# Performance work log

Hardware: AMD Instinct MI355X
Metric: run time of the kernel (lower is better)

Reference implementation:

```python
import jax, jax.numpy as jnp
import numpy as np

BN_EPS = 1e-5
STRIDE = 8  # encoder output stride -> upsample target is H*8


def conv2d(x, w, pad):
    return jax.lax.conv_general_dilated(
        x, w, (1, 1), [(pad, pad), (pad, pad)],
        dimension_numbers=('NCHW', 'OIHW', 'NCHW'))


def batchnorm(x, gamma, beta):
    # training-mode BN (batch statistics), matching a freshly-constructed torch module
    m = jnp.mean(x, axis=(0, 2, 3), keepdims=True)
    v = jnp.var(x, axis=(0, 2, 3), keepdims=True)
    xn = (x - m) * jax.lax.rsqrt(v + BN_EPS)
    return xn * gamma[None, :, None, None] + beta[None, :, None, None]


def setup_inputs() -> dict:
    key = jax.random.key(0)
    ks = jax.random.split(key, 8)
    B, C, H, W = 8, 256, 60, 60
    NC = 2
    return {
        'V_a': jax.random.normal(ks[0], (B, C, H, W), jnp.float32),
        'V_b': jax.random.normal(ks[1], (B, C, H, W), jnp.float32),
        'W_sim': jax.random.normal(ks[2], (C, C), jnp.float32) * 0.02,
        'gate_w': jax.random.normal(ks[3], (1, C, 1, 1), jnp.float32) * 0.01,
        'convA_w': jax.random.normal(ks[4], (C, 2 * C, 3, 3), jnp.float32) * 0.01,
        'convB_w': jax.random.normal(ks[5], (C, 2 * C, 3, 3), jnp.float32) * 0.01,
        'bnA_gamma': jnp.ones((C,), jnp.float32),
        'bnA_beta': jnp.zeros((C,), jnp.float32),
        'bnB_gamma': jnp.ones((C,), jnp.float32),
        'bnB_beta': jnp.zeros((C,), jnp.float32),
        'clsA_w': jax.random.normal(ks[6], (NC, C, 1, 1), jnp.float32) * 0.01,
        'clsA_b': jnp.zeros((NC,), jnp.float32),
        'clsB_w': jax.random.normal(ks[7], (NC, C, 1, 1), jnp.float32) * 0.01,
        'clsB_b': jnp.zeros((NC,), jnp.float32),
    }


def reference(V_a, V_b, W_sim, gate_w, convA_w, convB_w,
              bnA_gamma, bnA_beta, bnB_gamma, bnB_beta,
              clsA_w, clsA_b, clsB_w, clsB_b):
    B, C, H, W = V_a.shape
    HW = H * W
    out_h, out_w = H * STRIDE, W * STRIDE

    Va = V_a.reshape(B, C, HW)  # [B,C,HW_a]
    Vb = V_b.reshape(B, C, HW)  # [B,C,HW_b]

    # Linear on V_a^T: out[b,i,d] = sum_c Va[b,c,i] * W_sim[d,c]
    WVa = jnp.einsum('dc,bci->bdi', W_sim, Va)           # [B,C,HW_a]
    S = jnp.einsum('bdi,bdj->bij', WVa, Vb)              # [B,HW_a,HW_b]

    S_row = jax.nn.softmax(S, axis=1)                    # softmax over a-positions
    A_col = jax.nn.softmax(S, axis=2)                    # softmax over b-positions

    Z_b = jnp.einsum('bci,bij->bcj', Va, S_row).reshape(B, C, H, W)
    Z_a = jnp.einsum('bcj,bij->bci', Vb, A_col).reshape(B, C, H, W)

    mask_a = jax.nn.sigmoid(conv2d(Z_a, gate_w, 0))
    mask_b = jax.lax.stop_gradient(jax.nn.sigmoid(conv2d(Z_b, gate_w, 0)))
    Z_a = Z_a * mask_a
    Z_b = Z_b * mask_b

    Z_a = jnp.concatenate([Z_a, V_a], axis=1)            # [B,2C,H,W]
    Z_b = jnp.concatenate([Z_b, V_b], axis=1)

    Z_a = jax.nn.relu(batchnorm(conv2d(Z_a, convA_w, 1), bnA_gamma, bnA_beta))
    Z_b = jax.nn.relu(batchnorm(conv2d(Z_b, convB_w, 1), bnB_gamma, bnB_beta))

    x1 = conv2d(Z_a, clsA_w, 0) + clsA_b[None, :, None, None]
    x2 = conv2d(Z_b, clsB_w, 0) + clsB_b[None, :, None, None]

    NC = x1.shape[1]
    x1 = jax.image.resize(x1, (B, NC, out_h, out_w), method='bilinear')
    x2 = jax.image.resize(x2, (B, NC, out_h, out_w), method='bilinear')

    return jnp.stack([jax.nn.sigmoid(x1), jax.nn.sigmoid(x2)])  # [2,B,NC,out_h,out_w]
```

## Files before the change

kernel.cpp:

```cpp
#include <hip/hip_runtime.h>

#define C_CH   256
#define BATCH  8
#define HW     3600
#define CHW    (C_CH*HW)
#define NPIX   (BATCH*HW)
#define KCONV  4608
#define OHW    480
#define KP     3648
#define NROWP  3712
#define XPIX   3844
#define NT     57

typedef __attribute__((ext_vector_type(8))) short s16x8;
typedef __attribute__((ext_vector_type(4))) float f32x4;

__device__ __forceinline__ unsigned short f2bf(float f){
  unsigned int u = __float_as_uint(f);
  u += 0x7FFF + ((u>>16)&1);
  return (unsigned short)(u>>16);
}

__device__ __forceinline__ void gload16(const void* g, void* l){
  __builtin_amdgcn_global_load_lds((const __attribute__((address_space(1))) void*)g,
                                   (__attribute__((address_space(3))) void*)l, 16, 0, 0);
}

__device__ __forceinline__ void gemm_core(const char* a0, const char* b0,
                                          size_t lda, size_t ldb, int nkt,
                                          f32x4 acc[4][4]){
  __shared__ __align__(16) char LDS[32768];
  const int tid = threadIdx.x, l = tid & 63, w = tid >> 6;
  char* AsW = LDS + w*1024;
  char* BsW = LDS + 16384 + w*1024;
  const int arow = (w>>1)*64 + (l&15);
  const int brow = (w&1)*64 + (l&15);
  const int kc0 = (((l>>4)*16)      ) ^ ((l&7)<<4);
  const int kc1 = (((l>>4)*16) + 64 ) ^ ((l&7)<<4);
  const char* Ab = LDS;
  const char* Bb = LDS + 16384;
  for (int kt = 0; kt < nkt; ++kt){
#pragma unroll
    for (int i=0;i<4;i++){
      gload16(a0 + (size_t)(i*32)*lda + (size_t)kt*128, AsW + i*4096);
      gload16(b0 + (size_t)(i*32)*ldb + (size_t)kt*128, BsW + i*4096);
    }
    asm volatile("s_waitcnt vmcnt(0)" ::: "memory");
    __syncthreads();
    s16x8 af[4][2], bf[4][2];
#pragma unroll
    for (int f=0;f<4;f++){
      af[f][0] = *(const s16x8*)(Ab + (arow+f*16)*128 + kc0);
      af[f][1] = *(const s16x8*)(Ab + (arow+f*16)*128 + kc1);
      bf[f][0] = *(const s16x8*)(Bb + (brow+f*16)*128 + kc0);
      bf[f][1] = *(const s16x8*)(Bb + (brow+f*16)*128 + kc1);
    }
#pragma unroll
    for (int ks=0;ks<2;ks++)
#pragma unroll
      for (int fm=0;fm<4;fm++)
#pragma unroll
        for (int fn=0;fn<4;fn++)
          acc[fm][fn] = __builtin_amdgcn_mfma_f32_16x16x32_bf16(af[fm][ks], bf[fn][ks], acc[fm][fn], 0,0,0);
    __syncthreads();
  }
}

__global__ __launch_bounds__(256) void k_gemm_wva(const unsigned short* __restrict__ VaT,
                                                  const unsigned short* __restrict__ Wsim16,
                                                  unsigned short* __restrict__ WVaT){
  const int tid = threadIdx.x, l = tid&63, w = tid>>6;
  const int b = blockIdx.z;
  const int n0 = blockIdx.x*128, m0 = blockIdx.y*128;
  const int colS = ((tid&7)*16) ^ (((tid>>3)&7)<<4);
  const char* a0 = (const char*)(VaT + (size_t)b*NROWP*256) + (size_t)(m0 + (tid>>3))*512 + colS;
  const char* b0 = (const char*)Wsim16 + (size_t)(n0 + (tid>>3))*512 + colS;
  f32x4 acc[4][4] = {};
  gemm_core(a0, b0, 512, 512, 4, acc);
  unsigned short* ob = WVaT + (size_t)b*NROWP*256;
  const int mb = m0 + (w>>1)*64 + (l>>4)*4;
  const int nb = n0 + (w&1)*64 + (l&15);
#pragma unroll
  for (int fm=0;fm<4;fm++)
#pragma unroll
    for (int fn=0;fn<4;fn++){
      int n = nb + fn*16;
#pragma unroll
      for (int r=0;r<4;r++){
        int m = mb + fm*16 + r;
        if (m < HW) ob[(size_t)m*256 + n] = f2bf(acc[fm][fn][r]);
      }
    }
}

__global__ __launch_bounds__(256, 3) void flash_attn(const char* __restrict__ WVaT,
                                                  const char* __restrict__ VbT,
                                                  const char* __restrict__ VaT,
                                                  const char* __restrict__ Va16,
                                                  const char* __restrict__ Vb16,
                                                  const float* __restrict__ gw,
                                                  unsigned short* __restrict__ XtA,
                                                  unsigned short* __restrict__ XtB){
  __shared__ __align__(16) char LDS[40960];
  const int tid = threadIdx.x, l = tid&63, w = tid>>6;
  const int b = blockIdx.y, side = blockIdx.z;
  const size_t tOff = (size_t)b*NROWP*512;
  const size_t vOff = (size_t)b*256*KP*2;
  const char* QT = (side ? VbT  : WVaT) + tOff;
  const char* Kt = (side ? WVaT : VbT ) + tOff;
  const char* Vp = (side ? Va16 : Vb16) + vOff;
  const char* Vc = (side ? VbT  : VaT ) + tOff;
  unsigned short* Xt = (side ? XtB : XtA) + (size_t)b*XPIX*512;
  const int i0 = blockIdx.x*64;

  char* Kls = LDS;
  char* Pls = LDS + 32768;

  s16x8 q[8];
  {
    const char* qp = QT + (size_t)(i0 + w*16 + (l&15))*512 + (l>>4)*16;
#pragma unroll
    for (int ks=0;ks<8;ks++) q[ks] = *(const s16x8*)(qp + ks*64);
  }
  float gwv[4];
#pragma unroll
  for (int fn=0;fn<4;fn++) gwv[fn] = gw[w*64 + fn*16 + (l&15)];

  f32x4 acc[4][4] = {};
  f32x4 lac = {0.f,0.f,0.f,0.f};

  auto stageK = [&](int t){
    const char* src = Kt + (size_t)t*32768;
#pragma unroll
    for (int p=0;p<8;p++){
      int row = p*8 + (tid>>5), ch = tid&31;
      gload16(src + (size_t)row*512 + ((ch*16) ^ ((row&7)<<4)), Kls + p*4096 + tid*16);
    }
  };

  stageK(0);
  asm volatile("s_waitcnt vmcnt(0)" ::: "memory");
  __syncthreads();

  const char* vrow = Vp + (size_t)(w*64 + (l&15))*(KP*2) + (l>>4)*16;
  const int g = l>>4;

  for (int t=0; t<NT; ++t){
    s16x8 bv[2][4];
#pragma unroll
    for (int ks=0;ks<2;ks++)
#pragma unroll
      for (int fn=0;fn<4;fn++)
        bv[ks][fn] = *(const s16x8*)(vrow + (size_t)fn*16*(KP*2) + (size_t)t*128 + ks*64);
    f32x4 sac[4] = {};
#pragma unroll
    for (int ks=0;ks<8;ks++){
      s16x8 bk[4];
#pragma unroll
      for (int fn=0;fn<4;fn++){
        int row = fn*16 + (l&15);
        bk[fn] = *(const s16x8*)(Kls + row*512 + ((ks*64 + (l>>4)*16) ^ ((row&7)<<4)));
      }
#pragma unroll
      for (int fn=0;fn<4;fn++)
        sac[fn] = __builtin_amdgcn_mfma_f32_16x16x32_bf16(q[ks], bk[fn], sac[fn], 0,0,0);
    }
    const int j0 = t*64;
#pragma unroll
    for (int fn=0;fn<4;fn++){
      int col = fn*16 + (l&15);
      bool jv = (j0 + col) < HW;
#pragma unroll
      for (int r=0;r<4;r++){
        float e = jv ? __expf(sac[fn][r]) : 0.f;
        lac[r] += e;
        int row = w*16 + g*4 + r;
        *(unsigned short*)(Pls + row*128 + ((col*2) ^ (g<<5))) = f2bf(e);
      }
    }
    __syncthreads();
    if (t+1 < NT) stageK(t+1);
#pragma unroll
    for (int ks=0;ks<2;ks++){
      s16x8 ap[4];
#pragma unroll
      for (int fm=0;fm<4;fm++){
        int row = fm*16 + (l&15);
        ap[fm] = *(const s16x8*)(Pls + row*128 + ((ks*64 + (l>>4)*16) ^ ((((l&15)>>2)&3)<<5)));
      }
#pragma unroll
      for (int fm=0;fm<4;fm++)
#pragma unroll
        for (int fn=0;fn<4;fn++)
          acc[fm][fn] = __builtin_amdgcn_mfma_f32_16x16x32_bf16(ap[fm], bv[ks][fn], acc[fm][fn], 0,0,0);
    }
    asm volatile("s_waitcnt vmcnt(0)" ::: "memory");
    __syncthreads();
  }

  float* Lred = (float*)(LDS + 32768);
  float* Mls  = Lred + 64;
  float* Gp   = Mls + 64;
#pragma unroll
  for (int r=0;r<4;r++){
    float v = lac[r];
    v += __shfl_xor(v,1); v += __shfl_xor(v,2); v += __shfl_xor(v,4); v += __shfl_xor(v,8);
    if ((l&15)==0) Lred[w*16 + (l>>4)*4 + r] = 1.f / v;
  }
  __syncthreads();
#pragma unroll
  for (int fm=0;fm<4;fm++){
#pragma unroll
    for (int r=0;r<4;r++){
      float v = acc[fm][0][r]*gwv[0] + acc[fm][1][r]*gwv[1]
              + acc[fm][2][r]*gwv[2] + acc[fm][3][r]*gwv[3];
      v += __shfl_xor(v,1); v += __shfl_xor(v,2); v += __shfl_xor(v,4); v += __shfl_xor(v,8);
      if ((l&15)==0) Gp[w*64 + fm*16 + (l>>4)*4 + r] = v;
    }
  }
  __syncthreads();
  if (tid < 64){
    float gt = (Gp[tid] + Gp[64+tid] + Gp[128+tid] + Gp[192+tid]) * Lred[tid];
    Mls[tid] = 1.f/(1.f + __expf(-gt));
  }
  __syncthreads();
  char* Ost = LDS;
#pragma unroll
  for (int fm=0;fm<4;fm++){
    float4 li = *(const float4*)&Lred[fm*16 + (l>>4)*4];
    float4 mk = *(const float4*)&Mls [fm*16 + (l>>4)*4];
    float s0 = li.x*mk.x, s1 = li.y*mk.y, s2 = li.z*mk.z, s3 = li.w*mk.w;
#pragma unroll
    for (int fn=0;fn<4;fn++){
      int col = w*64 + fn*16 + (l&15);
      int row = fm*16 + (l>>4)*4;
      *(unsigned short*)(Ost + (row+0)*512 + col*2) = f2bf(acc[fm][fn][0]*s0);
      *(unsigned short*)(Ost + (row+1)*512 + col*2) = f2bf(acc[fm][fn][1]*s1);
      *(unsigned short*)(Ost + (row+2)*512 + col*2) = f2bf(acc[fm][fn][2]*s2);
      *(unsigned short*)(Ost + (row+3)*512 + col*2) = f2bf(acc[fm][fn][3]*s3);
    }
  }
  __syncthreads();
  {
    int row = tid>>2, ch = tid&3;
    int p = i0 + row;
    if (p < HW){
      int y = p/60, x = p - y*60;
      char* dst = (char*)Xt + (size_t)((y+1)*62 + (x+1))*1024 + ch*128;
      const char* osrc = Ost + row*512 + ch*128;
      const char* vsrc = Vc + (size_t)p*512 + ch*128;
#pragma unroll
      for (int q8=0;q8<8;q8++) *(uint4*)(dst + q8*16) = *(const uint4*)(osrc + q8*16);
#pragma unroll
      for (int q8=0;q8<8;q8++) *(uint4*)(dst + 512 + q8*16) = *(const uint4*)(vsrc + q8*16);
    }
  }
}

__global__ __launch_bounds__(256) void k_gemm_conv(const unsigned short* __restrict__ WcA,
                                                   const unsigned short* __restrict__ WcB,
                                                   const unsigned short* __restrict__ XtA,
                                                   const unsigned short* __restrict__ XtB,
                                                   float* __restrict__ Ra, float* __restrict__ Rb){
  __shared__ __align__(16) char LDS[32768];
  const int tid = threadIdx.x, l = tid&63, w = tid>>6;
  const unsigned short* Wc = blockIdx.z ? WcB : WcA;
  const unsigned short* Xt = blockIdx.z ? XtB : XtA;
  float* R = blockIdx.z ? Rb : Ra;
  const int n0 = blockIdx.x*128, m0 = blockIdx.y*128;
  const int colS = ((tid&7)*16) ^ (((tid>>3)&7)<<4);
  const int srow = tid>>3;
  const char* a0 = (const char*)Wc + (size_t)(m0+srow)*(KCONV*2) + colS;
  size_t bbase[4];
#pragma unroll
  for (int i=0;i<4;i++){
    int n = n0 + i*32 + srow;
    int bb = n/HW, p = n - bb*HW;
    int y = p/60, x = p - y*60;
    bbase[i] = ((size_t)bb*XPIX + (size_t)(y+1)*62 + (x+1))*1024 + colS;
  }
  char* AsW = LDS + w*1024;
  char* BsW = LDS + 16384 + w*1024;
  const int arow = (w>>1)*64 + (l&15);
  const int brow = (w&1)*64 + (l&15);
  const int kc0 = (((l>>4)*16)      ) ^ ((l&7)<<4);
  const int kc1 = (((l>>4)*16) + 64 ) ^ ((l&7)<<4);
  const char* Ab = LDS;
  const char* Bb = LDS + 16384;
  f32x4 acc[4][4] = {};
  for (int kt = 0; kt < 72; ++kt){
    const int sh = kt>>3;
    const int ci0b = (kt&7)*128;
    const int dy = sh/3 - 1, dx = (sh - (sh/3)*3) - 1;
    const int boff = (dy*62 + dx)*1024 + ci0b;
#pragma unroll
    for (int i=0;i<4;i++){
      gload16(a0 + (size_t)(i*32)*(KCONV*2) + (size_t)kt*128, AsW + i*4096);
      gload16((const char*)Xt + bbase[i] + boff, BsW + i*4096);
    }
    asm volatile("s_waitcnt vmcnt(0)" ::: "memory");
    __syncthreads();
    s16x8 af[4][2], bfr[4][2];
#pragma unroll
    for (int f=0;f<4;f++){
      af[f][0]  = *(const s16x8*)(Ab + (arow+f*16)*128 + kc0);
      af[f][1]  = *(const s16x8*)(Ab + (arow+f*16)*128 + kc1);
      bfr[f][0] = *(const s16x8*)(Bb + (brow+f*16)*128 + kc0);
      bfr[f][1] = *(const s16x8*)(Bb + (brow+f*16)*128 + kc1);
    }
#pragma unroll
    for (int ks=0;ks<2;ks++)
#pragma unroll
      for (int fm=0;fm<4;fm++)
#pragma unroll
        for (int fn=0;fn<4;fn++)
          acc[fm][fn] = __builtin_amdgcn_mfma_f32_16x16x32_bf16(af[fm][ks], bfr[fn][ks], acc[fm][fn], 0,0,0);
    __syncthreads();
  }
  const int mb = m0 + (w>>1)*64 + (l>>4)*4;
  const int nb = n0 + (w&1)*64 + (l&15);
#pragma unroll
  for (int fm=0;fm<4;fm++)
#pragma unroll
    for (int fn=0;fn<4;fn++){
      int n = nb + fn*16;
      int bb = n/HW, p = n - bb*HW;
      float* op = R + (size_t)bb*CHW + (size_t)(mb+fm*16)*HW + p;
#pragma unroll
      for (int r=0;r<4;r++) op[(size_t)r*HW] = acc[fm][fn][r];
    }
}

__global__ __launch_bounds__(256) void zerok(uint4* __restrict__ p, int n){
  int i = blockIdx.x*256 + threadIdx.x;
  if (i < n) p[i] = make_uint4(0,0,0,0);
}

__global__ __launch_bounds__(256) void convert_bf16(const float* __restrict__ in, unsigned short* __restrict__ out, int n){
  int i = blockIdx.x*256 + threadIdx.x;
  if (i < n) out[i] = f2bf(in[i]);
}

__global__ __launch_bounds__(256) void convw(const float* __restrict__ in, unsigned short* __restrict__ out){
  int idx = blockIdx.x*256 + threadIdx.x;
  int co = idx / KCONV;
  int kp = idx - co*KCONV;
  int sh = kp >> 9, ci = kp & 511;
  out[idx] = f2bf(in[co*KCONV + ci*9 + sh]);
}

__global__ __launch_bounds__(256) void convv(const float* __restrict__ in, unsigned short* __restrict__ out){
  int idx = blockIdx.x*256 + threadIdx.x;
  int row = idx / KP;
  int k = idx - row*KP;
  out[idx] = (k < HW) ? f2bf(in[(size_t)row*HW + k]) : 0;
}

__global__ __launch_bounds__(256) void convt(const float* __restrict__ in, unsigned short* __restrict__ out){
  __shared__ unsigned short T[64][66];
  const int b = blockIdx.y;
  const int i0 = blockIdx.x*64;
  const float* inb = in + (size_t)b*CHW;
  unsigned short* ob = out + (size_t)b*NROWP*256;
  for (int cc=0; cc<4; ++cc){
    __syncthreads();
    int i = i0 + (threadIdx.x & 63);
    int ic = i < HW ? i : HW-1;
#pragma unroll
    for (int r=0;r<16;r++){
      int cl = (threadIdx.x>>6)*16 + r;
      T[cl][threadIdx.x & 63] = f2bf(inb[(size_t)(cc*64+cl)*HW + ic]);
    }
    __syncthreads();
    int il = threadIdx.x>>2, seg = threadIdx.x&3;
    unsigned short tmp[16];
#pragma unroll
    for (int e=0;e<16;e++) tmp[e] = T[seg*16+e][il];
    *(s16x8*)(ob + (size_t)(i0+il)*256 + cc*64 + seg*16)     = *(const s16x8*)tmp;
    *(s16x8*)(ob + (size_t)(i0+il)*256 + cc*64 + seg*16 + 8) = *(const s16x8*)(tmp+8);
  }
}

__global__ __launch_bounds__(256) void bn_stats(const float* __restrict__ X, float* __restrict__ sums){
  int co = blockIdx.x;
  float s = 0.f, ss = 0.f;
  for (int i = threadIdx.x; i < NPIX; i += 256){
    int bi = i / HW, p = i - bi*HW;
    float v = X[(size_t)bi*CHW + (size_t)co*HW + p];
    s += v; ss += v*v;
  }
  __shared__ float rs[256], rss[256];
  rs[threadIdx.x] = s; rss[threadIdx.x] = ss; __syncthreads();
  for (int off=128; off>0; off>>=1){
    if (threadIdx.x < off){ rs[threadIdx.x] += rs[threadIdx.x+off]; rss[threadIdx.x] += rss[threadIdx.x+off]; }
    __syncthreads();
  }
  if (threadIdx.x==0){ sums[co] = rs[0]; sums[256+co] = rss[0]; }
}

__global__ __launch_bounds__(256) void cls_kernel(const float* __restrict__ R, const float* __restrict__ sums,
                                                  const float* __restrict__ gamma, const float* __restrict__ beta,
                                                  const float* __restrict__ cw, const float* __restrict__ cb,
                                                  float* __restrict__ Xout){
  __shared__ float red[2][4][64];
  int tx = threadIdx.x & 63, ty = threadIdx.x >> 6;
  int n = blockIdx.x*64 + tx;
  int bi = n / HW, p = n - bi*HW;
  float a0 = 0.f, a1 = 0.f;
  const float invN = 1.f/28800.f;
  for (int c = ty*64; c < ty*64+64; ++c){
    float mean = sums[c]*invN;
    float var  = sums[256+c]*invN - mean*mean;
    float sc   = gamma[c]*rsqrtf(var + 1e-5f);
    float shv  = beta[c] - mean*sc;
    float v = R[(size_t)bi*CHW + (size_t)c*HW + p]*sc + shv;
    v = fmaxf(v, 0.f);
    a0 += v*cw[c]; a1 += v*cw[256+c];
  }
  red[0][ty][tx] = a0; red[1][ty][tx] = a1; __syncthreads();
  if (ty==0){
    float r0 = red[0][0][tx]+red[0][1][tx]+red[0][2][tx]+red[0][3][tx] + cb[0];
    float r1 = red[1][0][tx]+red[1][1][tx]+red[1][2][tx]+red[1][3][tx] + cb[1];
    Xout[((size_t)bi*2 + 0)*HW + p] = r0;
    Xout[((size_t)bi*2 + 1)*HW + p] = r1;
  }
}

__global__ __launch_bounds__(256) void resize_kernel(const float* __restrict__ X1, const float* __restrict__ X2,
                                                     float* __restrict__ Out){
  int idx = blockIdx.x*256 + threadIdx.x;
  int ox = idx % OHW; int t = idx / OHW;
  int oy = t % OHW;  t /= OHW;
  int nc = t & 1;    t >>= 1;
  int bi = t & 7;    int s = t >> 3;
  const float* X = (s == 0) ? X1 : X2;
  float fy = (oy + 0.5f)*0.125f - 0.5f;
  float fx = (ox + 0.5f)*0.125f - 0.5f;
  float y0f = floorf(fy), x0f = floorf(fx);
  float wy = fy - y0f, wx = fx - x0f;
  int y0 = (int)y0f, x0 = (int)x0f;
  int y1 = min(max(y0+1,0),59), x1 = min(max(x0+1,0),59);
  y0 = min(max(y0,0),59); x0 = min(max(x0,0),59);
  const float* Xp = X + ((size_t)bi*2 + nc)*HW;
  float v00 = Xp[y0*60+x0], v01 = Xp[y0*60+x1];
  float v10 = Xp[y1*60+x0], v11 = Xp[y1*60+x1];
  float v = v00*(1.f-wy)*(1.f-wx) + v01*(1.f-wy)*wx + v10*wy*(1.f-wx) + v11*wy*wx;
  Out[idx] = 1.f/(1.f+__expf(-v));
}

extern "C" void kernel_launch(void* const* d_in, const int* in_sizes, int n_in,
                              void* d_out, int out_size, void* d_ws, size_t ws_size,
                              hipStream_t stream){
  const float* Va    = (const float*)d_in[0];
  const float* Vb    = (const float*)d_in[1];
  const float* Wsim  = (const float*)d_in[2];
  const float* gw    = (const float*)d_in[3];
  const float* cwA   = (const float*)d_in[4];
  const float* cwB   = (const float*)d_in[5];
  const float* gA    = (const float*)d_in[6];
  const float* bA    = (const float*)d_in[7];
  const float* gB    = (const float*)d_in[8];
  const float* bB    = (const float*)d_in[9];
  const float* clsAw = (const float*)d_in[10];
  const float* clsAb = (const float*)d_in[11];
  const float* clsBw = (const float*)d_in[12];
  const float* clsBb = (const float*)d_in[13];
  float* out = (float*)d_out;

  char* wsb = (char*)d_ws;
  size_t off = 0;
  auto alloc = [&](size_t bytes)->void*{
    void* pt = wsb + off;
    off += (bytes + 255) & ~(size_t)255;
    return pt;
  };
  unsigned short* Va16   = (unsigned short*)alloc((size_t)8*256*KP*2);
  unsigned short* Vb16   = (unsigned short*)alloc((size_t)8*256*KP*2);
  unsigned short* VaT16  = (unsigned short*)alloc((size_t)8*NROWP*256*2);
  unsigned short* VbT16  = (unsigned short*)alloc((size_t)8*NROWP*256*2);
  unsigned short* WVaT16 = (unsigned short*)alloc((size_t)8*NROWP*256*2);
  unsigned short* Wsim16 = (unsigned short*)alloc((size_t)256*256*2);
  unsigned short* WcA16  = (unsigned short*)alloc((size_t)256*KCONV*2);
  unsigned short* WcB16  = (unsigned short*)alloc((size_t)256*KCONV*2);
  unsigned short* XtA    = (unsigned short*)alloc((size_t)8*XPIX*512*2);
  unsigned short* XtB    = (unsigned short*)alloc((size_t)8*XPIX*512*2);
  float* sumsA= (float*)alloc(512*4);
  float* sumsB= (float*)alloc(512*4);
  float* Ra = (float*)Va16;
  float* Rb = (float*)VaT16;
  float* x1 = (float*)WVaT16;
  float* x2 = x1 + (size_t)BATCH*2*HW;

  zerok<<<dim3(15376), dim3(256), 0, stream>>>((uint4*)XtA, 3936256);
  convert_bf16<<<dim3(256), dim3(256), 0, stream>>>(Wsim, Wsim16, 65536);
  convw<<<dim3(4608), dim3(256), 0, stream>>>(cwA, WcA16);
  convw<<<dim3(4608), dim3(256), 0, stream>>>(cwB, WcB16);
  convv<<<dim3(29184), dim3(256), 0, stream>>>(Va, Va16);
  convv<<<dim3(29184), dim3(256), 0, stream>>>(Vb, Vb16);
  convt<<<dim3(57,8), dim3(256), 0, stream>>>(Va, VaT16);
  convt<<<dim3(57,8), dim3(256), 0, stream>>>(Vb, VbT16);
  k_gemm_wva<<<dim3(2,29,8), dim3(256), 0, stream>>>(VaT16, Wsim16, WVaT16);

  flash_attn<<<dim3(57,8,2), dim3(256), 0, stream>>>(
      (const char*)WVaT16, (const char*)VbT16, (const char*)VaT16,
      (const char*)Va16, (const char*)Vb16, gw, XtA, XtB);

  k_gemm_conv<<<dim3(225,2,2), dim3(256), 0, stream>>>(WcA16, WcB16, XtA, XtB, Ra, Rb);
  bn_stats<<<dim3(256), dim3(256), 0, stream>>>(Ra, sumsA);
  bn_stats<<<dim3(256), dim3(256), 0, stream>>>(Rb, sumsB);
  cls_kernel<<<dim3(450), dim3(256), 0, stream>>>(Ra, sumsA, gA, bA, clsAw, clsAb, x1);
  cls_kernel<<<dim3(450), dim3(256), 0, stream>>>(Rb, sumsB, gB, bB, clsBw, clsBb, x2);
  resize_kernel<<<dim3(28800), dim3(256), 0, stream>>>(x1, x2, out);
}
```

Baseline: 1.046 ms.

## Rewrite flash attention with 256-row query tiles, 32x32 MFMA and double-buffered K/V

```diff
diff --git a/kernel.cpp b/kernel.cpp
--- a/kernel.cpp
+++ b/kernel.cpp
@@ -8,12 +8,13 @@
 #define KCONV  4608
 #define OHW    480
 #define KP     3648
-#define NROWP  3712
+#define TR     3840
 #define XPIX   3844
-#define NT     57
+#define NTJ    57
 
 typedef __attribute__((ext_vector_type(8))) short s16x8;
 typedef __attribute__((ext_vector_type(4))) float f32x4;
+typedef __attribute__((ext_vector_type(16))) float f32x16;
 
 __device__ __forceinline__ unsigned short f2bf(float f){
   unsigned int u = __float_as_uint(f);
@@ -73,11 +74,11 @@
   const int b = blockIdx.z;
   const int n0 = blockIdx.x*128, m0 = blockIdx.y*128;
   const int colS = ((tid&7)*16) ^ (((tid>>3)&7)<<4);
-  const char* a0 = (const char*)(VaT + (size_t)b*NROWP*256) + (size_t)(m0 + (tid>>3))*512 + colS;
+  const char* a0 = (const char*)(VaT + (size_t)b*TR*256) + (size_t)(m0 + (tid>>3))*512 + colS;
   const char* b0 = (const char*)Wsim16 + (size_t)(n0 + (tid>>3))*512 + colS;
   f32x4 acc[4][4] = {};
   gemm_core(a0, b0, 512, 512, 4, acc);
-  unsigned short* ob = WVaT + (size_t)b*NROWP*256;
+  unsigned short* ob = WVaT + (size_t)b*TR*256;
   const int mb = m0 + (w>>1)*64 + (l>>4)*4;
   const int nb = n0 + (w&1)*64 + (l&15);
 #pragma unroll
@@ -93,166 +94,150 @@
     }
 }
 
-__global__ __launch_bounds__(256, 3) void flash_attn(const char* __restrict__ WVaT,
-                                                  const char* __restrict__ VbT,
-                                                  const char* __restrict__ VaT,
-                                                  const char* __restrict__ Va16,
-                                                  const char* __restrict__ Vb16,
-                                                  const float* __restrict__ gw,
-                                                  unsigned short* __restrict__ XtA,
-                                                  unsigned short* __restrict__ XtB){
-  __shared__ __align__(16) char LDS[40960];
-  const int tid = threadIdx.x, l = tid&63, w = tid>>6;
-  const int b = blockIdx.y, side = blockIdx.z;
-  const size_t tOff = (size_t)b*NROWP*512;
-  const size_t vOff = (size_t)b*256*KP*2;
+__global__ __launch_bounds__(512, 2) void flash2(const char* __restrict__ WVaT,
+                                                 const char* __restrict__ VbT,
+                                                 const char* __restrict__ VaT,
+                                                 const char* __restrict__ Va16,
+                                                 const char* __restrict__ Vb16,
+                                                 const float* __restrict__ gw,
+                                                 unsigned short* __restrict__ XtA,
+                                                 unsigned short* __restrict__ XtB){
+  extern __shared__ __align__(16) char LDS[];
+  const int tid = threadIdx.x;
+  const int l = tid & 63, w = tid >> 6;
+  const int lq = l & 31, g = l >> 5;
+  const int f = blockIdx.x;
+  const int b = f & 7;
+  const int k2 = f >> 3;
+  const int side = k2 / 15;
+  const int qb = k2 - side*15;
+  const size_t tOff = (size_t)b*TR*512;
+  const size_t vOff = (size_t)b*256*(KP*2);
   const char* QT = (side ? VbT  : WVaT) + tOff;
   const char* Kt = (side ? WVaT : VbT ) + tOff;
   const char* Vp = (side ? Va16 : Vb16) + vOff;
   const char* Vc = (side ? VbT  : VaT ) + tOff;
   unsigned short* Xt = (side ? XtB : XtA) + (size_t)b*XPIX*512;
-  const int i0 = blockIdx.x*64;
-
-  char* Kls = LDS;
-  char* Pls = LDS + 32768;
-
-  s16x8 q[8];
-  {
-    const char* qp = QT + (size_t)(i0 + w*16 + (l&15))*512 + (l>>4)*16;
-#pragma unroll
-    for (int ks=0;ks<8;ks++) q[ks] = *(const s16x8*)(qp + ks*64);
-  }
-  float gwv[4];
-#pragma unroll
-  for (int fn=0;fn<4;fn++) gwv[fn] = gw[w*64 + fn*16 + (l&15)];
-
-  f32x4 acc[4][4] = {};
-  f32x4 lac = {0.f,0.f,0.f,0.f};
-
-  auto stageK = [&](int t){
-    const char* src = Kt + (size_t)t*32768;
-#pragma unroll
-    for (int p=0;p<8;p++){
-      int row = p*8 + (tid>>5), ch = tid&31;
-      gload16(src + (size_t)row*512 + ((ch*16) ^ ((row&7)<<4)), Kls + p*4096 + tid*16);
-    }
-  };
-
-  stageK(0);
+  const int p0 = qb*256;
+
+#pragma unroll
+  for (int p=0;p<16;p++){
+    int row = p*16 + (tid>>5), ch = tid&31;
+    gload16(QT + (size_t)(p0+row)*512 + ((ch*16) ^ ((row&31)<<4)), LDS + p*8192 + tid*16);
+  }
   asm volatile("s_waitcnt vmcnt(0)" ::: "memory");
   __syncthreads();
-
-  const char* vrow = Vp + (size_t)(w*64 + (l&15))*(KP*2) + (l>>4)*16;
-  const int g = l>>4;
-
-  for (int t=0; t<NT; ++t){
-    s16x8 bv[2][4];
-#pragma unroll
-    for (int ks=0;ks<2;ks++)
-#pragma unroll
-      for (int fn=0;fn<4;fn++)
-        bv[ks][fn] = *(const s16x8*)(vrow + (size_t)fn*16*(KP*2) + (size_t)t*128 + ks*64);
-    f32x4 sac[4] = {};
-#pragma unroll
-    for (int ks=0;ks<8;ks++){
-      s16x8 bk[4];
-#pragma unroll
-      for (int fn=0;fn<4;fn++){
-        int row = fn*16 + (l&15);
-        bk[fn] = *(const s16x8*)(Kls + row*512 + ((ks*64 + (l>>4)*16) ^ ((row&7)<<4)));
+  s16x8 qf[16];
+#pragma unroll
+  for (int st=0; st<16; ++st)
+    qf[st] = *(const s16x8*)(LDS + (size_t)(w*32+lq)*512 + ((st*32 + g*16) ^ (lq<<4)));
+  __syncthreads();
+
+  auto stageKV = [&](int t, int o){
+    char* Kd = LDS + o*32768;
+    char* Vd = LDS + 65536 + o*32768;
+#pragma unroll
+    for (int p=0;p<4;p++){
+      int row = p*16 + (tid>>5), ch = tid&31;
+      gload16(Kt + (size_t)(t*64+row)*512 + ((ch*16) ^ ((row&31)<<4)), Kd + p*8192 + tid*16);
+    }
+#pragma unroll
+    for (int p=0;p<4;p++){
+      int c = p*64 + (tid>>3), ch = tid&7;
+      gload16(Vp + (size_t)c*(KP*2) + (size_t)t*128 + ((ch*16) ^ ((c&7)<<4)), Vd + p*8192 + tid*16);
+    }
+  };
+
+  stageKV(0, 0);
+  asm volatile("s_waitcnt vmcnt(0)" ::: "memory");
+  __syncthreads();
+
+  f32x16 acc[8] = {};
+  float lac = 0.f;
+
+  for (int t=0; t<NTJ; ++t){
+    const int o = t&1;
+    if (t+1 < NTJ) stageKV(t+1, o^1);
+    const char* Kb = LDS + o*32768;
+    const char* Vbuf = LDS + 65536 + o*32768;
+#pragma unroll
+    for (int jt=0;jt<2;jt++){
+      f32x16 sac = {};
+#pragma unroll
+      for (int st=0;st<16;st++){
+        s16x8 kf = *(const s16x8*)(Kb + (size_t)(jt*32+lq)*512 + ((st*32+g*16) ^ (lq<<4)));
+        sac = __builtin_amdgcn_mfma_f32_32x32x16_bf16(kf, qf[st], sac, 0,0,0);
       }
-#pragma unroll
-      for (int fn=0;fn<4;fn++)
-        sac[fn] = __builtin_amdgcn_mfma_f32_16x16x32_bf16(q[ks], bk[fn], sac[fn], 0,0,0);
-    }
-    const int j0 = t*64;
-#pragma unroll
-    for (int fn=0;fn<4;fn++){
-      int col = fn*16 + (l&15);
-      bool jv = (j0 + col) < HW;
-#pragma unroll
-      for (int r=0;r<4;r++){
-        float e = jv ? __expf(sac[fn][r]) : 0.f;
-        lac[r] += e;
-        int row = w*16 + g*4 + r;
-        *(unsigned short*)(Pls + row*128 + ((col*2) ^ (g<<5))) = f2bf(e);
+      float pe[16];
+      const int jb = t*64 + jt*32 + 4*g;
+#pragma unroll
+      for (int r=0;r<16;r++){
+        int j = jb + (r&3) + 8*(r>>2);
+        float e = (j < HW) ? __expf(sac[r]) : 0.f;
+        lac += e; pe[r] = e;
       }
-    }
-    __syncthreads();
-    if (t+1 < NT) stageK(t+1);
-#pragma unroll
-    for (int ks=0;ks<2;ks++){
-      s16x8 ap[4];
-#pragma unroll
-      for (int fm=0;fm<4;fm++){
-        int row = fm*16 + (l&15);
-        ap[fm] = *(const s16x8*)(Pls + row*128 + ((ks*64 + (l>>4)*16) ^ ((((l&15)>>2)&3)<<5)));
+#pragma unroll
+      for (int kp=0;kp<2;kp++){
+        unsigned u0,u1,u2,u3;
+        asm("v_cvt_pk_bf16_f32 %0, %1, %2" : "=v"(u0) : "v"(pe[8*kp+0]), "v"(pe[8*kp+1]));
+        asm("v_cvt_pk_bf16_f32 %0, %1, %2" : "=v"(u1) : "v"(pe[8*kp+2]), "v"(pe[8*kp+3]));
+        asm("v_cvt_pk_bf16_f32 %0, %1, %2" : "=v"(u2) : "v"(pe[8*kp+4]), "v"(pe[8*kp+5]));
+        asm("v_cvt_pk_bf16_f32 %0, %1, %2" : "=v"(u3) : "v"(pe[8*kp+6]), "v"(pe[8*kp+7]));
+        unsigned s0 = (unsigned)__shfl_xor((int)u0,32), s1 = (unsigned)__shfl_xor((int)u1,32);
+        unsigned s2 = (unsigned)__shfl_xor((int)u2,32), s3 = (unsigned)__shfl_xor((int)u3,32);
+        uint4 pw;
+        pw.x = g ? s2 : u0;  pw.y = g ? s3 : u1;
+        pw.z = g ? u2 : s0;  pw.w = g ? u3 : s1;
+        s16x8 pf = *(s16x8*)&pw;
+        const int ks = jt*2 + kp;
+#pragma unroll
+        for (int ct=0;ct<8;ct++){
+          s16x8 vf = *(const s16x8*)(Vbuf + (size_t)(ct*32+lq)*128 + ((ks*32+g*16) ^ ((lq&7)<<4)));
+          acc[ct] = __builtin_amdgcn_mfma_f32_32x32x16_bf16(pf, vf, acc[ct], 0,0,0);
+        }
       }
-#pragma unroll
-      for (int fm=0;fm<4;fm++)
-#pragma unroll
-        for (int fn=0;fn<4;fn++)
-          acc[fm][fn] = __builtin_amdgcn_mfma_f32_16x16x32_bf16(ap[fm], bv[ks][fn], acc[fm][fn], 0,0,0);
     }
     asm volatile("s_waitcnt vmcnt(0)" ::: "memory");
     __syncthreads();
   }
 
-  float* Lred = (float*)(LDS + 32768);
-  float* Mls  = Lred + 64;
-  float* Gp   = Mls + 64;
-#pragma unroll
-  for (int r=0;r<4;r++){
-    float v = lac[r];
-    v += __shfl_xor(v,1); v += __shfl_xor(v,2); v += __shfl_xor(v,4); v += __shfl_xor(v,8);
-    if ((l&15)==0) Lred[w*16 + (l>>4)*4 + r] = 1.f / v;
-  }
+  float lt = lac + __shfl_xor(lac, 32);
+  float invl = 1.f/lt;
+  float* Linv = (float*)(LDS + 131072);
+  if (!g) Linv[w*32 + lq] = invl;
+  float gwv[8];
+#pragma unroll
+  for (int ct=0;ct<8;ct++) gwv[ct] = gw[ct*32 + lq];
   __syncthreads();
-#pragma unroll
-  for (int fm=0;fm<4;fm++){
-#pragma unroll
-    for (int r=0;r<4;r++){
-      float v = acc[fm][0][r]*gwv[0] + acc[fm][1][r]*gwv[1]
-              + acc[fm][2][r]*gwv[2] + acc[fm][3][r]*gwv[3];
-      v += __shfl_xor(v,1); v += __shfl_xor(v,2); v += __shfl_xor(v,4); v += __shfl_xor(v,8);
-      if ((l&15)==0) Gp[w*64 + fm*16 + (l>>4)*4 + r] = v;
-    }
+  unsigned short* Ost = (unsigned short*)LDS;
+#pragma unroll
+  for (int r=0;r<16;r++){
+    float p = 0.f;
+#pragma unroll
+    for (int ct=0;ct<8;ct++) p += acc[ct][r]*gwv[ct];
+    p += __shfl_xor(p,1); p += __shfl_xor(p,2); p += __shfl_xor(p,4);
+    p += __shfl_xor(p,8); p += __shfl_xor(p,16);
+    int ql = 4*g + (r&3) + 8*(r>>2);
+    float il = Linv[w*32 + ql];
+    float mk = 1.f/(1.f + __expf(-p*il));
+    float sc = il*mk;
+#pragma unroll
+    for (int ct=0;ct<8;ct++)
+      Ost[(size_t)(w*32+ql)*256 + ct*32 + lq] = f2bf(acc[ct][r]*sc);
   }
   __syncthreads();
-  if (tid < 64){
-    float gt = (Gp[tid] + Gp[64+tid] + Gp[128+tid] + Gp[192+tid]) * Lred[tid];
-    Mls[tid] = 1.f/(1.f + __expf(-gt));
-  }
-  __syncthreads();
-  char* Ost = LDS;
-#pragma unroll
-  for (int fm=0;fm<4;fm++){
-    float4 li = *(const float4*)&Lred[fm*16 + (l>>4)*4];
-    float4 mk = *(const float4*)&Mls [fm*16 + (l>>4)*4];
-    float s0 = li.x*mk.x, s1 = li.y*mk.y, s2 = li.z*mk.z, s3 = li.w*mk.w;
-#pragma unroll
-    for (int fn=0;fn<4;fn++){
-      int col = w*64 + fn*16 + (l&15);
-      int row = fm*16 + (l>>4)*4;
-      *(unsigned short*)(Ost + (row+0)*512 + col*2) = f2bf(acc[fm][fn][0]*s0);
-      *(unsigned short*)(Ost + (row+1)*512 + col*2) = f2bf(acc[fm][fn][1]*s1);
-      *(unsigned short*)(Ost + (row+2)*512 + col*2) = f2bf(acc[fm][fn][2]*s2);
-      *(unsigned short*)(Ost + (row+3)*512 + col*2) = f2bf(acc[fm][fn][3]*s3);
-    }
-  }
-  __syncthreads();
-  {
-    int row = tid>>2, ch = tid&3;
-    int p = i0 + row;
+#pragma unroll
+  for (int pass=0; pass<2; ++pass){
+    int unit = tid + pass*512;
+    int row = unit>>2, qt = unit&3;
+    int p = p0 + row;
     if (p < HW){
       int y = p/60, x = p - y*60;
-      char* dst = (char*)Xt + (size_t)((y+1)*62 + (x+1))*1024 + ch*128;
-      const char* osrc = Ost + row*512 + ch*128;
-      const char* vsrc = Vc + (size_t)p*512 + ch*128;
-#pragma unroll
-      for (int q8=0;q8<8;q8++) *(uint4*)(dst + q8*16) = *(const uint4*)(osrc + q8*16);
-#pragma unroll
-      for (int q8=0;q8<8;q8++) *(uint4*)(dst + 512 + q8*16) = *(const uint4*)(vsrc + q8*16);
+      char* dst = (char*)Xt + (size_t)((y+1)*62 + (x+1))*1024 + qt*256;
+      const char* src = (qt < 2) ? (const char*)LDS + (size_t)row*512 + qt*256
+                                 : Vc + (size_t)p*512 + (qt-2)*256;
+#pragma unroll
+      for (int q8=0;q8<16;q8++) *(uint4*)(dst + q8*16) = *(const uint4*)(src + q8*16);
     }
   }
 }
@@ -361,7 +346,7 @@
   const int b = blockIdx.y;
   const int i0 = blockIdx.x*64;
   const float* inb = in + (size_t)b*CHW;
-  unsigned short* ob = out + (size_t)b*NROWP*256;
+  unsigned short* ob = out + (size_t)b*TR*256;
   for (int cc=0; cc<4; ++cc){
     __syncthreads();
     int i = i0 + (threadIdx.x & 63);
@@ -476,9 +461,9 @@
   };
   unsigned short* Va16   = (unsigned short*)alloc((size_t)8*256*KP*2);
   unsigned short* Vb16   = (unsigned short*)alloc((size_t)8*256*KP*2);
-  unsigned short* VaT16  = (unsigned short*)alloc((size_t)8*NROWP*256*2);
-  unsigned short* VbT16  = (unsigned short*)alloc((size_t)8*NROWP*256*2);
-  unsigned short* WVaT16 = (unsigned short*)alloc((size_t)8*NROWP*256*2);
+  unsigned short* VaT16  = (unsigned short*)alloc((size_t)8*TR*256*2);
+  unsigned short* VbT16  = (unsigned short*)alloc((size_t)8*TR*256*2);
+  unsigned short* WVaT16 = (unsigned short*)alloc((size_t)8*TR*256*2);
   unsigned short* Wsim16 = (unsigned short*)alloc((size_t)256*256*2);
   unsigned short* WcA16  = (unsigned short*)alloc((size_t)256*KCONV*2);
   unsigned short* WcB16  = (unsigned short*)alloc((size_t)256*KCONV*2);
@@ -501,7 +486,7 @@
   convt<<<dim3(57,8), dim3(256), 0, stream>>>(Vb, VbT16);
   k_gemm_wva<<<dim3(2,29,8), dim3(256), 0, stream>>>(VaT16, Wsim16, WVaT16);
 
-  flash_attn<<<dim3(57,8,2), dim3(256), 0, stream>>>(
+  flash2<<<dim3(240), dim3(512), 132096, stream>>>(
       (const char*)WVaT16, (const char*)VbT16, (const char*)VaT16,
       (const char*)Va16, (const char*)Vb16, gw, XtA, XtB);
 
```

After: 843.5 us. 1.24x faster.
